# Optimization experiments

Measured on AMD Instinct MI355X. Metric: run time of the kernel, lower is better.

Reference implementation:

```python
import jax, jax.numpy as jnp
import numpy as np

B, N, D, O, K, E = 16, 10000, 128, 64, 3, 160000


def setup_inputs() -> dict:
    key = jax.random.key(0)
    k1, k2, k3, k4, k5 = jax.random.split(key, 5)
    x = jax.random.normal(k1, (B, N, D), dtype=jnp.float32)
    W = jax.random.normal(k2, (K, D, O), dtype=jnp.float32) * (1.0 / np.sqrt(D))
    sup_vals = jax.random.uniform(k3, (K, E), dtype=jnp.float32)
    sup_row = jax.random.randint(k4, (K, E), 0, N, dtype=jnp.int32)
    sup_col = jax.random.randint(k5, (K, E), 0, N, dtype=jnp.int32)
    return {"x": x, "W": W, "sup_vals": sup_vals, "sup_row": sup_row, "sup_col": sup_col}


def reference(x, W, sup_vals, sup_row, sup_col):
    # x: [B, N, D]; W: [K, D, O]; supports as COO edge lists per support.
    # dropout=0.0 (keep_prob=1) -> identity; act=None -> identity; agg='concat'.
    num_nodes = x.shape[1]
    num_supports = W.shape[0]
    outs = []
    for i in range(num_supports):
        # dense feature transform, laid out node-major for the SpMM: [N, B, O]
        pre = jnp.einsum('bnd,do->nbo', x, W[i])
        # SpMM: out[r] += A[r,c] * pre[c]  via gather + segment_sum
        gathered = pre[sup_col[i]] * sup_vals[i][:, None, None]  # [E, B, O]
        agg = jax.ops.segment_sum(gathered, sup_row[i], num_segments=num_nodes)  # [N, B, O]
        outs.append(jnp.transpose(agg, (1, 0, 2)))  # [B, N, O]
    return jnp.concatenate(outs, axis=-1)  # [B, N, O*K]
```

## Files before the change

### kernel.cpp

```cpp
#include <hip/hip_runtime.h>
#include <hip/hip_bf16.h>

constexpr int B = 16, N = 10000, D = 128, O = 64, K = 3, E = 160000;
constexpr int BO = B * O;
constexpr int KO = K * O;
constexpr int NPB = 8;
constexpr int G = 8;
constexpr int ROWS = 8;
constexpr int NCH = N / ROWS;

using short8  = __attribute__((ext_vector_type(8))) short;
using floatx4 = __attribute__((ext_vector_type(4))) float;
struct U4 { unsigned a, b, c, d; };

__device__ __forceinline__ float bf2f(unsigned short u) {
  return __uint_as_float(((unsigned int)u) << 16);
}
__device__ __forceinline__ unsigned short f2bf(float f) {
  return (unsigned short)((__float_as_uint(f) + 0x8000u) >> 16);
}
__device__ __forceinline__ unsigned pkbf(float lo, float hi) {
  return ((__float_as_uint(lo) + 0x8000u) >> 16) |
         ((__float_as_uint(hi) + 0x8000u) & 0xFFFF0000u);
}

__global__ void wpack_kernel(const float* __restrict__ w, unsigned short* __restrict__ wp) {
  const int i = blockIdx.x * 64 + threadIdx.x;
  if (i >= K * 16 * 64) return;
  const int lane = i & 63;
  const int dd = (i >> 6) & 3;
  const int t4 = (i >> 8) & 3;
  const int k  = i >> 10;
  const int o  = t4 * 16 + (lane & 15);
  const int d0 = dd * 32 + (lane >> 4) * 8;
  unsigned short* dst = wp + (size_t)i * 8;
#pragma unroll
  for (int j = 0; j < 8; ++j)
    dst[j] = f2bf(w[((size_t)k * D + d0 + j) * O + o]);
}

__global__ __launch_bounds__(192) void gemm_mfma_kernel(
    const float* __restrict__ x, const unsigned short* __restrict__ wpk,
    unsigned short* __restrict__ pre, int kBase)
{
  const int t = threadIdx.x;
  const int kloc = t >> 6;
  const int k = kBase + kloc;
  const int lane = t & 63;
  const int col  = lane & 15;
  const int quad = lane >> 4;

  short8 wfr[4][4];
#pragma unroll
  for (int t4 = 0; t4 < 4; ++t4)
#pragma unroll
    for (int dd = 0; dd < 4; ++dd)
      wfr[t4][dd] = *(const short8*)(wpk + (size_t)(((k * 4 + t4) * 4 + dd) * 64 + lane) * 8);

  const int n0 = blockIdx.x * NPB;
  const float* xbase = x + (size_t)col * N * D;

  for (int nn = 0; nn < NPB; ++nn) {
    const int n = n0 + nn;
    const float* xp = xbase + (size_t)n * D + quad * 8;
    short8 xfr[4];
#pragma unroll
    for (int dd = 0; dd < 4; ++dd) {
      const float4 lo = *(const float4*)(xp + dd * 32);
      const float4 hi = *(const float4*)(xp + dd * 32 + 4);
      U4 u;
      u.a = pkbf(lo.x, lo.y); u.b = pkbf(lo.z, lo.w);
      u.c = pkbf(hi.x, hi.y); u.d = pkbf(hi.z, hi.w);
      xfr[dd] = __builtin_bit_cast(short8, u);
    }

    floatx4 acc[4] = {};
#pragma unroll
    for (int dd = 0; dd < 4; ++dd)
#pragma unroll
      for (int t4 = 0; t4 < 4; ++t4)
        acc[t4] = __builtin_amdgcn_mfma_f32_16x16x32_bf16(wfr[t4][dd], xfr[dd], acc[t4], 0, 0, 0);

    unsigned short* pp = pre + (((size_t)kloc * N + n) << 10) + col * 64 + quad * 4;
#pragma unroll
    for (int t4 = 0; t4 < 4; ++t4) {
      uint2 pk2;
      pk2.x = pkbf(acc[t4][0], acc[t4][1]);
      pk2.y = pkbf(acc[t4][2], acc[t4][3]);
      *(uint2*)(pp + t4 * 16) = pk2;
    }
  }
}

__global__ void hist_kernel(const int* __restrict__ row, int* __restrict__ cnt) {
  const int i = blockIdx.x * 256 + threadIdx.x;
  if (i >= K * E) return;
  const int k = i / E;
  atomicAdd(&cnt[k * N + row[i]], 1);
}

__global__ __launch_bounds__(1024) void scan_kernel(int* __restrict__ cnt,
                                                    int* __restrict__ offs) {
  const int k = blockIdx.x;
  const int t = threadIdx.x;
  const int lane = t & 63, wid = t >> 6;
  __shared__ int wt[16];
  __shared__ int sbase;
  if (t == 0) { sbase = 0; offs[k * (N + 1)] = 0; }
  __syncthreads();

  for (int c0 = 0; c0 < N; c0 += 1024) {
    const int i = c0 + t;
    const int v = (i < N) ? cnt[k * N + i] : 0;
    int incl = v;
#pragma unroll
    for (int st = 1; st < 64; st <<= 1) {
      const int u = __shfl_up(incl, st, 64);
      if (lane >= st) incl += u;
    }
    if (lane == 63) wt[wid] = incl;
    __syncthreads();
    if (wid == 0) {
      int wv = (lane < 16) ? wt[lane] : 0;
#pragma unroll
      for (int st = 1; st < 16; st <<= 1) {
        const int u = __shfl_up(wv, st, 64);
        if (lane >= st) wv += u;
      }
      if (lane < 16) wt[lane] = wv;
    }
    __syncthreads();
    const int base = sbase + ((wid > 0) ? wt[wid - 1] : 0);
    if (i < N) {
      offs[k * (N + 1) + i + 1] = base + incl;
      cnt[k * N + i] = base + incl - v;
    }
    __syncthreads();
    if (t == 0) sbase += wt[15];
    __syncthreads();
  }
}

__global__ void scatter_kernel(const int* __restrict__ row, const int* __restrict__ col,
                               const float* __restrict__ vals,
                               int* __restrict__ cursor, int* __restrict__ scol,
                               float* __restrict__ sval) {
  const int i = blockIdx.x * 256 + threadIdx.x;
  if (i >= K * E) return;
  const int k = i / E;
  const int pos = atomicAdd(&cursor[k * N + row[i]], 1);
  scol[k * E + pos] = col[i];
  sval[k * E + pos] = vals[i];
}

__global__ __launch_bounds__(64) void spmm_kernel(
    const unsigned short* __restrict__ pre, const int* __restrict__ offs,
    const int* __restrict__ scol, const float* __restrict__ sval,
    float* __restrict__ out, int kBase)
{
  const int bid = blockIdx.x;
  const int g   = bid & 7;
  const int t2  = bid >> 3;
  const int nc  = t2 % NCH;
  const int kloc = t2 / NCH;
  const int k = kBase + kloc;
  const int lane = threadIdx.x;

  const int bo = g * 128 + 2 * lane;
  const int b = bo >> 6;
  const int o = bo & 63;
  const unsigned short* pk = pre + (((size_t)kloc * N) << 10) + bo;
  const int* cj = scol + (size_t)k * E;
  const float* vj = sval + (size_t)k * E;
  const int* op = offs + k * (N + 1) + nc * ROWS;

  for (int r = 0; r < ROWS; ++r) {
    const int j0 = __builtin_amdgcn_readfirstlane(op[r]);
    const int j1 = __builtin_amdgcn_readfirstlane(op[r + 1]);
    float a0 = 0.f, a1 = 0.f;
    int j = j0;
    for (; j + 7 < j1; j += 8) {
      unsigned u[8]; float v[8];
#pragma unroll
      for (int i = 0; i < 8; ++i) {
        const int c = __builtin_amdgcn_readfirstlane(cj[j + i]);
        u[i] = *(const unsigned*)(pk + ((size_t)c << 10));
        v[i] = vj[j + i];
      }
#pragma unroll
      for (int i = 0; i < 8; ++i) {
        a0 += v[i] * bf2f((unsigned short)(u[i] & 0xFFFFu));
        a1 += v[i] * bf2f((unsigned short)(u[i] >> 16));
      }
    }
    for (; j < j1; ++j) {
      const int c = __builtin_amdgcn_readfirstlane(cj[j]);
      const float v = vj[j];
      const unsigned u = *(const unsigned*)(pk + ((size_t)c << 10));
      a0 += v * bf2f((unsigned short)(u & 0xFFFFu));
      a1 += v * bf2f((unsigned short)(u >> 16));
    }
    const int n = nc * ROWS + r;
    float2 st; st.x = a0; st.y = a1;
    *(float2*)(out + ((size_t)b * N + n) * KO + (size_t)k * O + o) = st;
  }
}

extern "C" void kernel_launch(void* const* d_in, const int* in_sizes, int n_in,
                              void* d_out, int out_size, void* d_ws, size_t ws_size,
                              hipStream_t stream) {
  const float* x    = (const float*)d_in[0];
  const float* w    = (const float*)d_in[1];
  const float* vals = (const float*)d_in[2];
  const int* row    = (const int*)d_in[3];
  const int* col    = (const int*)d_in[4];
  float* out        = (float*)d_out;

  char* p = (char*)d_ws;
  int* offs = (int*)p;            p += ((size_t)K * (N + 1) * 4 + 15) & ~(size_t)15;
  int* cnt  = (int*)p;            p += (size_t)K * N * 4;
  int* scol = (int*)p;            p += (size_t)K * E * 4;
  float* sval = (float*)p;        p += (size_t)K * E * 4;
  unsigned short* wpk = (unsigned short*)p; p += (size_t)K * 16 * 64 * 8 * 2;
  unsigned short* pre = (unsigned short*)p;
  const size_t fixed = (size_t)(p - (char*)d_ws);
  const size_t preFull = (size_t)K * N * BO * 2;
  const bool full = ws_size >= fixed + preFull;

  hipMemsetAsync(cnt, 0, (size_t)K * N * 4, stream);

  wpack_kernel<<<48, 64, 0, stream>>>(w, wpk);
  const int eb = (K * E + 255) / 256;
  hist_kernel<<<eb, 256, 0, stream>>>(row, cnt);
  scan_kernel<<<K, 1024, 0, stream>>>(cnt, offs);
  scatter_kernel<<<eb, 256, 0, stream>>>(row, col, vals, cnt, scol, sval);

  if (full) {
    gemm_mfma_kernel<<<N / NPB, 64 * K, 0, stream>>>(x, wpk, pre, 0);
    spmm_kernel<<<K * NCH * G, 64, 0, stream>>>(pre, offs, scol, sval, out, 0);
  } else {
    for (int k = 0; k < K; ++k) {
      gemm_mfma_kernel<<<N / NPB, 64, 0, stream>>>(x, wpk, pre, k);
      spmm_kernel<<<NCH * G, 64, 0, stream>>>(pre, offs, scol, sval, out, k);
    }
  }
  (void)in_sizes; (void)n_in; (void)out_size;
}
```

Measured before the change: 396.9 us.

## Persistent SpMM with XCD-aware slots, node-major GEMM tiling and hardware bf16 packing

The SpMM becomes a persistent grid of 2048 blocks of 4 waves. Slots are assigned so that the 8 column-groups of a row chunk map by blockIdx&7, aiming to keep each group's gathered slice in one XCD's L2, and row offsets are preloaded. Outputs are written with nontemporal stores. The GEMM now tiles 16 nodes by 4 batches per block instead of 16 batches by 8 nodes, and uses v_cvt_pk_bf16_f32 for packing, which changes rounding semantics slightly (RNE versus add-and-truncate).

```diff
diff --git a/kernel.cpp b/kernel.cpp
--- a/kernel.cpp
+++ b/kernel.cpp
@@ -4,13 +4,17 @@
 constexpr int B = 16, N = 10000, D = 128, O = 64, K = 3, E = 160000;
 constexpr int BO = B * O;
 constexpr int KO = K * O;
-constexpr int NPB = 8;
+constexpr int BSPL = 4;
+constexpr int BPB  = B / BSPL;
 constexpr int G = 8;
 constexpr int ROWS = 8;
 constexpr int NCH = N / ROWS;
+constexpr int SPMM_BLOCKS = 2048;
+constexpr int SLOTS_PER_XCD = (SPMM_BLOCKS / 8) * 4;
 
 using short8  = __attribute__((ext_vector_type(8))) short;
 using floatx4 = __attribute__((ext_vector_type(4))) float;
+using f32x2   = __attribute__((ext_vector_type(2))) float;
 struct U4 { unsigned a, b, c, d; };
 
 __device__ __forceinline__ float bf2f(unsigned short u) {
@@ -19,9 +23,10 @@
 __device__ __forceinline__ unsigned short f2bf(float f) {
   return (unsigned short)((__float_as_uint(f) + 0x8000u) >> 16);
 }
-__device__ __forceinline__ unsigned pkbf(float lo, float hi) {
-  return ((__float_as_uint(lo) + 0x8000u) >> 16) |
-         ((__float_as_uint(hi) + 0x8000u) & 0xFFFF0000u);
+__device__ __forceinline__ unsigned cvtpk(float lo, float hi) {
+  unsigned r;
+  asm("v_cvt_pk_bf16_f32 %0, %1, %2" : "=v"(r) : "v"(lo), "v"(hi));
+  return r;
 }
 
 __global__ void wpack_kernel(const float* __restrict__ w, unsigned short* __restrict__ wp) {
@@ -57,20 +62,21 @@
     for (int dd = 0; dd < 4; ++dd)
       wfr[t4][dd] = *(const short8*)(wpk + (size_t)(((k * 4 + t4) * 4 + dd) * 64 + lane) * 8);
 
-  const int n0 = blockIdx.x * NPB;
-  const float* xbase = x + (size_t)col * N * D;
-
-  for (int nn = 0; nn < NPB; ++nn) {
-    const int n = n0 + nn;
-    const float* xp = xbase + (size_t)n * D + quad * 8;
+  const int n0 = (blockIdx.x / BSPL) * 16;
+  const int b0 = (blockIdx.x % BSPL) * BPB;
+  const int n  = n0 + col;
+
+  for (int bb = 0; bb < BPB; ++bb) {
+    const int b = b0 + bb;
+    const float* xp = x + ((size_t)b * N + n) * D + quad * 8;
     short8 xfr[4];
 #pragma unroll
     for (int dd = 0; dd < 4; ++dd) {
       const float4 lo = *(const float4*)(xp + dd * 32);
       const float4 hi = *(const float4*)(xp + dd * 32 + 4);
       U4 u;
-      u.a = pkbf(lo.x, lo.y); u.b = pkbf(lo.z, lo.w);
-      u.c = pkbf(hi.x, hi.y); u.d = pkbf(hi.z, hi.w);
+      u.a = cvtpk(lo.x, lo.y); u.b = cvtpk(lo.z, lo.w);
+      u.c = cvtpk(hi.x, hi.y); u.d = cvtpk(hi.z, hi.w);
       xfr[dd] = __builtin_bit_cast(short8, u);
     }
 
@@ -81,12 +87,12 @@
       for (int t4 = 0; t4 < 4; ++t4)
         acc[t4] = __builtin_amdgcn_mfma_f32_16x16x32_bf16(wfr[t4][dd], xfr[dd], acc[t4], 0, 0, 0);
 
-    unsigned short* pp = pre + (((size_t)kloc * N + n) << 10) + col * 64 + quad * 4;
+    unsigned short* pp = pre + (((size_t)kloc * N + n) << 10) + b * 64 + quad * 4;
 #pragma unroll
     for (int t4 = 0; t4 < 4; ++t4) {
       uint2 pk2;
-      pk2.x = pkbf(acc[t4][0], acc[t4][1]);
-      pk2.y = pkbf(acc[t4][2], acc[t4][3]);
+      pk2.x = cvtpk(acc[t4][0], acc[t4][1]);
+      pk2.y = cvtpk(acc[t4][2], acc[t4][3]);
       *(uint2*)(pp + t4 * 16) = pk2;
     }
   }
@@ -153,56 +159,66 @@
   sval[k * E + pos] = vals[i];
 }
 
-__global__ __launch_bounds__(64) void spmm_kernel(
+__global__ __launch_bounds__(256, 8) void spmm_kernel(
     const unsigned short* __restrict__ pre, const int* __restrict__ offs,
     const int* __restrict__ scol, const float* __restrict__ sval,
-    float* __restrict__ out, int kBase)
+    float* __restrict__ out, int kBase, int kCount)
 {
-  const int bid = blockIdx.x;
-  const int g   = bid & 7;
-  const int t2  = bid >> 3;
-  const int nc  = t2 % NCH;
-  const int kloc = t2 / NCH;
-  const int k = kBase + kloc;
-  const int lane = threadIdx.x;
+  const int g    = blockIdx.x & 7;
+  const int slot = (blockIdx.x >> 3) * 4 + (threadIdx.x >> 6);
+  const int lane = threadIdx.x & 63;
 
   const int bo = g * 128 + 2 * lane;
   const int b = bo >> 6;
   const int o = bo & 63;
-  const unsigned short* pk = pre + (((size_t)kloc * N) << 10) + bo;
-  const int* cj = scol + (size_t)k * E;
-  const float* vj = sval + (size_t)k * E;
-  const int* op = offs + k * (N + 1) + nc * ROWS;
-
-  for (int r = 0; r < ROWS; ++r) {
-    const int j0 = __builtin_amdgcn_readfirstlane(op[r]);
-    const int j1 = __builtin_amdgcn_readfirstlane(op[r + 1]);
-    float a0 = 0.f, a1 = 0.f;
-    int j = j0;
-    for (; j + 7 < j1; j += 8) {
-      unsigned u[8]; float v[8];
-#pragma unroll
-      for (int i = 0; i < 8; ++i) {
-        const int c = __builtin_amdgcn_readfirstlane(cj[j + i]);
-        u[i] = *(const unsigned*)(pk + ((size_t)c << 10));
-        v[i] = vj[j + i];
+  const int total = kCount * NCH;
+
+  for (int c = slot; c < total; c += SLOTS_PER_XCD) {
+    const int kloc = c / NCH;
+    const int nc   = c - kloc * NCH;
+    const int k = kBase + kloc;
+
+    const unsigned short* pk = pre + (((size_t)kloc * N) << 10) + bo;
+    const int* cj = scol + (size_t)k * E;
+    const float* vj = sval + (size_t)k * E;
+    const int* op = offs + k * (N + 1) + nc * ROWS;
+
+    int ofs[ROWS + 1];
+#pragma unroll
+    for (int r = 0; r <= ROWS; ++r) ofs[r] = __builtin_amdgcn_readfirstlane(op[r]);
+
+#pragma unroll
+    for (int r = 0; r < ROWS; ++r) {
+      const int j0 = ofs[r];
+      const int j1 = ofs[r + 1];
+      float a0 = 0.f, a1 = 0.f;
+      int j = j0;
+      for (; j + 7 < j1; j += 8) {
+        unsigned u[8]; float v[8];
+#pragma unroll
+        for (int i = 0; i < 8; ++i) {
+          const int c2 = __builtin_amdgcn_readfirstlane(cj[j + i]);
+          u[i] = *(const unsigned*)(pk + ((size_t)c2 << 10));
+          v[i] = vj[j + i];
+        }
+#pragma unroll
+        for (int i = 0; i < 8; ++i) {
+          a0 += v[i] * bf2f((unsigned short)(u[i] & 0xFFFFu));
+          a1 += v[i] * bf2f((unsigned short)(u[i] >> 16));
+        }
       }
-#pragma unroll
-      for (int i = 0; i < 8; ++i) {
-        a0 += v[i] * bf2f((unsigned short)(u[i] & 0xFFFFu));
-        a1 += v[i] * bf2f((unsigned short)(u[i] >> 16));
+      for (; j < j1; ++j) {
+        const int c2 = __builtin_amdgcn_readfirstlane(cj[j]);
+        const float v = vj[j];
+        const unsigned u = *(const unsigned*)(pk + ((size_t)c2 << 10));
+        a0 += v * bf2f((unsigned short)(u & 0xFFFFu));
+        a1 += v * bf2f((unsigned short)(u >> 16));
       }
-    }
-    for (; j < j1; ++j) {
-      const int c = __builtin_amdgcn_readfirstlane(cj[j]);
-      const float v = vj[j];
-      const unsigned u = *(const unsigned*)(pk + ((size_t)c << 10));
-      a0 += v * bf2f((unsigned short)(u & 0xFFFFu));
-      a1 += v * bf2f((unsigned short)(u >> 16));
-    }
-    const int n = nc * ROWS + r;
-    float2 st; st.x = a0; st.y = a1;
-    *(float2*)(out + ((size_t)b * N + n) * KO + (size_t)k * O + o) = st;
+      const int n = nc * ROWS + r;
+      f32x2 st; st.x = a0; st.y = a1;
+      __builtin_nontemporal_store(st,
+          (f32x2*)(out + ((size_t)b * N + n) * KO + (size_t)k * O + o));
+    }
   }
 }
 
@@ -236,12 +252,12 @@
   scatter_kernel<<<eb, 256, 0, stream>>>(row, col, vals, cnt, scol, sval);
 
   if (full) {
-    gemm_mfma_kernel<<<N / NPB, 64 * K, 0, stream>>>(x, wpk, pre, 0);
-    spmm_kernel<<<K * NCH * G, 64, 0, stream>>>(pre, offs, scol, sval, out, 0);
+    gemm_mfma_kernel<<<(N / 16) * BSPL, 64 * K, 0, stream>>>(x, wpk, pre, 0);
+    spmm_kernel<<<SPMM_BLOCKS, 256, 0, stream>>>(pre, offs, scol, sval, out, 0, K);
   } else {
     for (int k = 0; k < K; ++k) {
-      gemm_mfma_kernel<<<N / NPB, 64, 0, stream>>>(x, wpk, pre, k);
-      spmm_kernel<<<NCH * G, 64, 0, stream>>>(pre, offs, scol, sval, out, k);
+      gemm_mfma_kernel<<<(N / 16) * BSPL, 64, 0, stream>>>(x, wpk, pre, k);
+      spmm_kernel<<<SPMM_BLOCKS, 256, 0, stream>>>(pre, offs, scol, sval, out, k, 1);
     }
   }
   (void)in_sizes; (void)n_in; (void)out_size;
```

After: 431.0 us. +8.6%, slower.
